# Kernel tuning notes

Hardware: AMD Instinct MI355X
Metric: run time of the kernel (lower is better)

## Reference

```python
import jax, jax.numpy as jnp
import numpy as np


def _normalize(x):
    # F.normalize(x, dim=-1): x / max(||x||_2, eps)
    n = jnp.linalg.norm(x, axis=-1, keepdims=True)
    return x / jnp.maximum(n, 1e-12)


def _clip_loss(i_sh, t_sh, scale, y):
    # Faithful, vectorized version of CLIP.forward (y: [B,1] int labels).
    i_n = _normalize(i_sh)
    t_n = _normalize(t_sh)
    logit_i2t = (i_n @ t_n.T) * scale            # [B,B]
    logit_t2i = t_n @ i_n.T                      # NOTE: no scale, as in source
    bs = i_sh.shape[0]
    yv = y.reshape(-1)                           # [B]
    # y.expand(bs,bs).T with y [bs,1] -> base[k,j] = y[j]
    base = jnp.broadcast_to(yv[None, :], (bs, bs)).astype(i_sh.dtype)
    flipped = jnp.where(base == 0, 1.0, 0.0)     # the inner loop flips 0<->nonzero
    label = jnp.where(yv[:, None] == 0, flipped, base)
    q = jax.nn.softmax(label / label.sum(axis=-1, keepdims=True), axis=-1)
    lq = jnp.log(q)
    lp1 = jax.nn.log_softmax(logit_i2t, axis=-1)
    lp2 = jax.nn.log_softmax(logit_t2i, axis=-1)
    # F.kl_div(input=log_pred, target, 'batchmean') = sum(target*(log(target)-input))/bs
    kl_p1_q = jnp.sum(q * (lq - lp1)) / bs
    kl_q_p1 = jnp.sum(jnp.exp(lp1) * (lp1 - lq)) / bs
    kl_p2_q = jnp.sum(q * (lq - lp2)) / bs
    kl_q_p2 = jnp.sum(jnp.exp(lp2) * (lp2 - lq)) / bs
    return (kl_p1_q + kl_q_p1 + kl_p2_q + kl_q_p2) / 4.0


def _forward(i, t, y, l1_w, l1_b, l2_w, l2_b, l3_w, l3_b, tl1_w, tl1_b, tl2_w, tl2_b,
             isp_w, isp_b, ish_w, ish_b, tsh_w, tsh_b, tsp_w, tsp_b,
             c1_w, c1_b, c2_w, c2_b, c3_w, c3_b, c4_w, c4_b, scale1, scale2):
    # ImgEncoder MLP head (penet backbone replaced by pooled 2048-d features;
    # dropout = identity, eval semantics)
    fi = jax.nn.relu(i @ l1_w.T + l1_b)
    fi = jax.nn.relu(fi @ l2_w.T + l2_b)
    fi = fi @ l3_w.T + l3_b                       # [B,128]
    # TabEncoder
    ft = jax.nn.relu(t @ tl1_w.T + tl1_b)
    ft = ft @ tl2_w.T + tl2_b                     # [B,128]
    loss1 = _clip_loss(fi, ft, jnp.exp(scale1), y)
    # SS heads
    i_sp = fi @ isp_w.T + isp_b
    i_sh = fi @ ish_w.T + ish_b
    t_sh = ft @ tsh_w.T + tsh_b
    t_sp = ft @ tsp_w.T + tsp_b
    # Separate: mean of Frobenius norms of BxB cross-Grams
    loss_sp = (jnp.linalg.norm(t_sp @ t_sh.T) + jnp.linalg.norm(i_sp @ i_sh.T)) / 2.0
    loss_sh = _clip_loss(i_sh, t_sh, jnp.exp(scale2), y)
    loss = (loss_sp + loss_sh + loss1) / 3.0
    i_sp_out = i_sp @ c1_w.T + c1_b
    i_sh_out = i_sh @ c2_w.T + c2_b
    t_sh_out = t_sh @ c3_w.T + c3_b
    t_sp_out = t_sp @ c4_w.T + c4_b
    return (loss, i_sp_out, i_sh_out, t_sp_out, t_sh_out)


def setup_inputs() -> dict:
    key = jax.random.key(0)
    ks = jax.random.split(key, 20)
    B = 4096

    def lin(k, out_d, in_d):  # kaiming-normal fan_out, relu
        return jax.random.normal(k, (out_d, in_d), jnp.float32) * np.sqrt(2.0 / out_d)

    log_scale = jnp.asarray(np.log(1.0 / 0.07), jnp.float32)
    return {
        'i': jax.random.normal(ks[0], (B, 2048), jnp.float32),
        't': jax.random.normal(ks[1], (B, 49), jnp.float32),
        'y': jax.random.randint(ks[2], (B, 1), 0, 2, jnp.int64 if jax.config.read('jax_enable_x64') else jnp.int32),
        'l1_w': lin(ks[3], 512, 2048), 'l1_b': jnp.zeros((512,), jnp.float32),
        'l2_w': lin(ks[4], 256, 512), 'l2_b': jnp.zeros((256,), jnp.float32),
        'l3_w': lin(ks[5], 128, 256), 'l3_b': jnp.zeros((128,), jnp.float32),
        'tl1_w': lin(ks[6], 128, 49), 'tl1_b': jnp.zeros((128,), jnp.float32),
        'tl2_w': lin(ks[7], 128, 128), 'tl2_b': jnp.zeros((128,), jnp.float32),
        'isp_w': lin(ks[8], 128, 128), 'isp_b': jnp.zeros((128,), jnp.float32),
        'ish_w': lin(ks[9], 128, 128), 'ish_b': jnp.zeros((128,), jnp.float32),
        'tsh_w': lin(ks[10], 128, 128), 'tsh_b': jnp.zeros((128,), jnp.float32),
        'tsp_w': lin(ks[11], 128, 128), 'tsp_b': jnp.zeros((128,), jnp.float32),
        'c1_w': lin(ks[12], 1, 128), 'c1_b': jnp.zeros((1,), jnp.float32),
        'c2_w': lin(ks[13], 1, 128), 'c2_b': jnp.zeros((1,), jnp.float32),
        'c3_w': lin(ks[14], 1, 128), 'c3_b': jnp.zeros((1,), jnp.float32),
        'c4_w': lin(ks[15], 1, 128), 'c4_b': jnp.zeros((1,), jnp.float32),
        'scale1': log_scale, 'scale2': log_scale,
    }


def reference(i, t, y, l1_w, l1_b, l2_w, l2_b, l3_w, l3_b, tl1_w, tl1_b, tl2_w, tl2_b,
              isp_w, isp_b, ish_w, ish_b, tsh_w, tsh_b, tsp_w, tsp_b,
              c1_w, c1_b, c2_w, c2_b, c3_w, c3_b, c4_w, c4_b, scale1, scale2):
    return _forward(i, t, y, l1_w, l1_b, l2_w, l2_b, l3_w, l3_b, tl1_w, tl1_b, tl2_w, tl2_b,
                    isp_w, isp_b, ish_w, ish_b, tsh_w, tsh_b, tsp_w, tsp_b,
                    c1_w, c1_b, c2_w, c2_b, c3_w, c3_b, c4_w, c4_b, scale1, scale2)
```

## Files before the change

kernel.cpp:

```cpp
#include <hip/hip_runtime.h>
#include <math.h>

#define BSZ 4096

typedef __attribute__((ext_vector_type(8))) short bf16x8;
typedef __attribute__((ext_vector_type(4))) float f32x4;

#define ST_ROW 0
#define ST_COL 786432
#define ST_T   1572864
#define ST_FLOATS 1589248

__device__ __forceinline__ unsigned short f2b(float f) {
    unsigned u = __float_as_uint(f);
    u = u + 0x7fffu + ((u >> 16) & 1u);
    return (unsigned short)(u >> 16);
}
__device__ __forceinline__ float b2f(unsigned short s) {
    return __uint_as_float(((unsigned)s) << 16);
}

__global__ void cast_kernel(const float* __restrict__ x, unsigned short* __restrict__ o, int n) {
    int i = (blockIdx.x * 256 + threadIdx.x) * 4;
    if (i >= n) return;
    float4 v = *(const float4*)(x + i);
    ushort4 r;
    r.x = f2b(v.x); r.y = f2b(v.y); r.z = f2b(v.z); r.w = f2b(v.w);
    *(ushort4*)(o + i) = r;
}

__global__ void cast_w_kernel(const float* __restrict__ l1, const float* __restrict__ l2,
                              const float* __restrict__ l3, const float* __restrict__ tl2,
                              const float* __restrict__ isp, const float* __restrict__ ish,
                              const float* __restrict__ tsh, const float* __restrict__ tsp,
                              unsigned short* __restrict__ o) {
    int i = (blockIdx.x * 256 + threadIdx.x) * 4;
    if (i >= 1294336) return;
    const float* src; int off;
    if (i < 1048576)      { src = l1;  off = 0; }
    else if (i < 1179648) { src = l2;  off = 1048576; }
    else if (i < 1212416) { src = l3;  off = 1179648; }
    else if (i < 1228800) { src = tl2; off = 1212416; }
    else if (i < 1245184) { src = isp; off = 1228800; }
    else if (i < 1261568) { src = ish; off = 1245184; }
    else if (i < 1277952) { src = tsh; off = 1261568; }
    else                  { src = tsp; off = 1277952; }
    float4 v = *(const float4*)(src + (i - off));
    ushort4 r;
    r.x = f2b(v.x); r.y = f2b(v.y); r.z = f2b(v.z); r.w = f2b(v.w);
    *(ushort4*)(o + i) = r;
}

__global__ void gemm_small(const float* __restrict__ A, const float* __restrict__ W,
                           const float* __restrict__ bias, unsigned short* __restrict__ C,
                           int M, int N, int K, int relu) {
    __shared__ float As[16][65];
    __shared__ float Ws[16][65];
    const int tx = threadIdx.x, ty = threadIdx.y;
    const int tid = ty * 16 + tx;
    const int m0 = blockIdx.y * 64, n0 = blockIdx.x * 64;
    float acc[4][4] = {};
    const int lrow = tid >> 2;
    const int lkb = (tid & 3) * 4;
    for (int k0 = 0; k0 < K; k0 += 16) {
#pragma unroll
        for (int u = 0; u < 4; ++u) {
            int k = k0 + lkb + u;
            As[lkb + u][lrow] = (k < K) ? A[(size_t)(m0 + lrow) * K + k] : 0.0f;
            Ws[lkb + u][lrow] = (k < K) ? W[(size_t)(n0 + lrow) * K + k] : 0.0f;
        }
        __syncthreads();
#pragma unroll
        for (int kk = 0; kk < 16; ++kk) {
            float av[4], bv[4];
#pragma unroll
            for (int i = 0; i < 4; ++i) av[i] = As[kk][ty * 4 + i];
#pragma unroll
            for (int j = 0; j < 4; ++j) bv[j] = Ws[kk][tx * 4 + j];
#pragma unroll
            for (int i = 0; i < 4; ++i)
#pragma unroll
                for (int j = 0; j < 4; ++j) acc[i][j] += av[i] * bv[j];
        }
        __syncthreads();
    }
#pragma unroll
    for (int i = 0; i < 4; ++i)
#pragma unroll
        for (int j = 0; j < 4; ++j) {
            int n = n0 + tx * 4 + j;
            float v = acc[i][j] + bias[n];
            if (relu) v = fmaxf(v, 0.0f);
            C[(size_t)(m0 + ty * 4 + i) * N + n] = f2b(v);
        }
}

__device__ __forceinline__ void gemm_body(const unsigned short* __restrict__ A,
                                          const unsigned short* __restrict__ W,
                                          const float* __restrict__ bias,
                                          unsigned short* __restrict__ Cb,
                                          float* __restrict__ Cf,
                                          int N, int K, int relu, int bx, int by,
                                          short* As, short* Bs) {
    const int tid = threadIdx.x;
    const int w = tid >> 6, lane = tid & 63, quad = lane >> 4, l15 = lane & 15;
    const int m0 = by * 128, n0 = bx * 128;
    const int rw = (w >> 1) * 64, cw = (w & 1) * 64;
    f32x4 acc[4][4];
#pragma unroll
    for (int i = 0; i < 4; ++i)
#pragma unroll
        for (int j = 0; j < 4; ++j) acc[i][j] = (f32x4){0.f, 0.f, 0.f, 0.f};

    for (int k0 = 0; k0 < K; k0 += 64) {
#pragma unroll
        for (int r = 0; r < 4; ++r) {
            int idx = r * 256 + tid;
            int row = idx >> 3, cbp = idx & 7;
            int col = ((cbp ^ (row & 7)) << 3);
            *(bf16x8*)&As[row * 64 + cbp * 8] = *(const bf16x8*)&A[(size_t)(m0 + row) * K + k0 + col];
            *(bf16x8*)&Bs[row * 64 + cbp * 8] = *(const bf16x8*)&W[(size_t)(n0 + row) * K + k0 + col];
        }
        __syncthreads();
#pragma unroll
        for (int kb = 0; kb < 2; ++kb) {
            bf16x8 af[4], bfr[4];
            int cb = kb * 4 + quad;
#pragma unroll
            for (int i = 0; i < 4; ++i) {
                int row = rw + i * 16 + l15;
                af[i] = *(const bf16x8*)&As[row * 64 + ((cb ^ (row & 7)) << 3)];
            }
#pragma unroll
            for (int j = 0; j < 4; ++j) {
                int row = cw + j * 16 + l15;
                bfr[j] = *(const bf16x8*)&Bs[row * 64 + ((cb ^ (row & 7)) << 3)];
            }
#pragma unroll
            for (int i = 0; i < 4; ++i)
#pragma unroll
                for (int j = 0; j < 4; ++j)
                    acc[i][j] = __builtin_amdgcn_mfma_f32_16x16x32_bf16(af[i], bfr[j], acc[i][j], 0, 0, 0);
        }
        __syncthreads();
    }
#pragma unroll
    for (int j = 0; j < 4; ++j) {
        int n = n0 + cw + j * 16 + l15;
        float bv = bias[n];
#pragma unroll
        for (int i = 0; i < 4; ++i) {
#pragma unroll
            for (int r = 0; r < 4; ++r) {
                int m = m0 + rw + i * 16 + quad * 4 + r;
                float v = acc[i][j][r] + bv;
                if (relu) v = fmaxf(v, 0.f);
                if (Cb) Cb[(size_t)m * N + n] = f2b(v);
                if (Cf) Cf[(size_t)m * N + n] = v;
            }
        }
    }
}

__global__ __launch_bounds__(256) void mfma_gemm(const unsigned short* __restrict__ A,
                                                 const unsigned short* __restrict__ W,
                                                 const float* __restrict__ bias,
                                                 unsigned short* __restrict__ Cb,
                                                 float* __restrict__ Cf, int N, int K, int relu) {
    __shared__ alignas(16) short As[128 * 64];
    __shared__ alignas(16) short Bs[128 * 64];
    gemm_body(A, W, bias, Cb, Cf, N, K, relu, blockIdx.x, blockIdx.y, As, Bs);
}

__global__ __launch_bounds__(256) void mfma_heads(const unsigned short* __restrict__ FIb,
                                                  const unsigned short* __restrict__ FTb,
                                                  const unsigned short* __restrict__ Wisp,
                                                  const unsigned short* __restrict__ Wish,
                                                  const unsigned short* __restrict__ Wtsh,
                                                  const unsigned short* __restrict__ Wtsp,
                                                  const float* __restrict__ bisp, const float* __restrict__ bish,
                                                  const float* __restrict__ btsh, const float* __restrict__ btsp,
                                                  float* __restrict__ ISP, float* __restrict__ ISH,
                                                  float* __restrict__ TSH, float* __restrict__ TSP) {
    __shared__ alignas(16) short As[128 * 64];
    __shared__ alignas(16) short Bs[128 * 64];
    int z = blockIdx.z;
    const unsigned short* A = (z < 2) ? FIb : FTb;
    const unsigned short* W = z == 0 ? Wisp : z == 1 ? Wish : z == 2 ? Wtsh : Wtsp;
    const float* b = z == 0 ? bisp : z == 1 ? bish : z == 2 ? btsh : btsp;
    float* C = z == 0 ? ISP : z == 1 ? ISH : z == 2 ? TSH : TSP;
    gemm_body(A, W, b, nullptr, C, 128, 128, 0, 0, blockIdx.y, As, Bs);
}

__global__ void rownorm4(const unsigned short* __restrict__ fi, const unsigned short* __restrict__ ft,
                         const float* __restrict__ ish, const float* __restrict__ tsh,
                         unsigned short* __restrict__ fin, unsigned short* __restrict__ ftn,
                         unsigned short* __restrict__ ishn, unsigned short* __restrict__ tshn) {
    int z = blockIdx.y;
    int m = blockIdx.x * 256 + threadIdx.x;
    const unsigned short* sb = (z == 0) ? fi : ft;
    const float* sf = (z == 2) ? ish : tsh;
    unsigned short* dst = z == 0 ? fin : z == 1 ? ftn : z == 2 ? ishn : tshn;
    float ss = 0.f;
    if (z < 2) {
        for (int u = 0; u < 128; u += 8) {
            bf16x8 v = *(const bf16x8*)&sb[(size_t)m * 128 + u];
#pragma unroll
            for (int e = 0; e < 8; ++e) { float f = b2f((unsigned short)v[e]); ss += f * f; }
        }
    } else {
        for (int u = 0; u < 128; u += 4) {
            float4 v = *(const float4*)&sf[(size_t)m * 128 + u];
            ss += v.x * v.x + v.y * v.y + v.z * v.z + v.w * v.w;
        }
    }
    float inv = 1.f / fmaxf(sqrtf(ss), 1e-12f);
    if (z < 2) {
        for (int u = 0; u < 128; u += 8) {
            bf16x8 v = *(const bf16x8*)&sb[(size_t)m * 128 + u];
            ushort4 o0, o1;
            o0.x = f2b(b2f((unsigned short)v[0]) * inv); o0.y = f2b(b2f((unsigned short)v[1]) * inv);
            o0.z = f2b(b2f((unsigned short)v[2]) * inv); o0.w = f2b(b2f((unsigned short)v[3]) * inv);
            o1.x = f2b(b2f((unsigned short)v[4]) * inv); o1.y = f2b(b2f((unsigned short)v[5]) * inv);
            o1.z = f2b(b2f((unsigned short)v[6]) * inv); o1.w = f2b(b2f((unsigned short)v[7]) * inv);
            *(ushort4*)&dst[(size_t)m * 128 + u] = o0;
            *(ushort4*)&dst[(size_t)m * 128 + u + 4] = o1;
        }
    } else {
        for (int u = 0; u < 128; u += 4) {
            float4 v = *(const float4*)&sf[(size_t)m * 128 + u];
            ushort4 o;
            o.x = f2b(v.x * inv); o.y = f2b(v.y * inv); o.z = f2b(v.z * inv); o.w = f2b(v.w * inv);
            *(ushort4*)&dst[(size_t)m * 128 + u] = o;
        }
    }
}

__global__ __launch_bounds__(256) void clip_mfma(const unsigned short* __restrict__ In1,
                                                 const unsigned short* __restrict__ Tn1,
                                                 const unsigned short* __restrict__ In2,
                                                 const unsigned short* __restrict__ Tn2,
                                                 const int* __restrict__ y,
                                                 const float* __restrict__ scale_log1,
                                                 const float* __restrict__ scale_log2,
                                                 float* __restrict__ st1, float* __restrict__ st2) {
    __shared__ alignas(16) short As[128 * 128];
    __shared__ alignas(16) short Bs[128 * 128];
    const int z = blockIdx.z;
    const unsigned short* In = z ? In2 : In1;
    const unsigned short* Tn = z ? Tn2 : Tn1;
    const float* scale_log = z ? scale_log2 : scale_log1;
    float* st = z ? st2 : st1;
    const int tid = threadIdx.x;
    const int w = tid >> 6, lane = tid & 63, quad = lane >> 4, l15 = lane & 15;
    const int bx = blockIdx.x, by = blockIdx.y;
    const int r0 = by * 128, c0 = bx * 128;
    const int rw = (w >> 1) * 64, cw = (w & 1) * 64;
#pragma unroll
    for (int r = 0; r < 8; ++r) {
        int idx = r * 256 + tid;
        int row = idx >> 4, cbp = idx & 15;
        int col = ((cbp ^ (row & 7)) << 3);
        *(bf16x8*)&As[row * 128 + cbp * 8] = *(const bf16x8*)&In[(size_t)(r0 + row) * 128 + col];
        *(bf16x8*)&Bs[row * 128 + cbp * 8] = *(const bf16x8*)&Tn[(size_t)(c0 + row) * 128 + col];
    }
    __syncthreads();
    f32x4 acc[4][4];
#pragma unroll
    for (int i = 0; i < 4; ++i)
#pragma unroll
        for (int j = 0; j < 4; ++j) acc[i][j] = (f32x4){0.f, 0.f, 0.f, 0.f};
#pragma unroll
    for (int kb = 0; kb < 4; ++kb) {
        bf16x8 af[4], bfr[4];
        int cb = kb * 4 + quad;
#pragma unroll
        for (int i = 0; i < 4; ++i) {
            int row = rw + i * 16 + l15;
            af[i] = *(const bf16x8*)&As[row * 128 + ((cb ^ (row & 7)) << 3)];
        }
#pragma unroll
        for (int j = 0; j < 4; ++j) {
            int row = cw + j * 16 + l15;
            bfr[j] = *(const bf16x8*)&Bs[row * 128 + ((cb ^ (row & 7)) << 3)];
        }
#pragma unroll
        for (int i = 0; i < 4; ++i)
#pragma unroll
            for (int j = 0; j < 4; ++j)
                acc[i][j] = __builtin_amdgcn_mfma_f32_16x16x32_bf16(af[i], bfr[j], acc[i][j], 0, 0, 0);
    }

    const float s = expf(scale_log[0]);
    int yrow[4][4]; float mrow[4][4];
    int ycol[4];    float mcol[4];
#pragma unroll
    for (int i = 0; i < 4; ++i)
#pragma unroll
        for (int r = 0; r < 4; ++r) {
            int yy = y[r0 + rw + i * 16 + quad * 4 + r];
            yrow[i][r] = yy; mrow[i][r] = (yy == 0) ? 1.f : 0.f;
        }
#pragma unroll
    for (int j = 0; j < 4; ++j) {
        int yy = y[c0 + cw + j * 16 + l15];
        ycol[j] = yy; mcol[j] = (yy == 0) ? 1.f : 0.f;
    }
    float rZ[4][4] = {}, rF[4][4] = {}, rW[4][4] = {};
    float cZ[4] = {}, cE[4] = {}, cW[4] = {};
    float aAll = 0.f, aC0 = 0.f, aR0 = 0.f, aRC = 0.f;
#pragma unroll
    for (int i = 0; i < 4; ++i)
#pragma unroll
        for (int r = 0; r < 4; ++r) {
            float mr = mrow[i][r];
            int yr = yrow[i][r];
#pragma unroll
            for (int j = 0; j < 4; ++j) {
                float S = acc[i][j][r];
                float L = s * S;
                float e1 = __expf(L);
                float e2 = __expf(S);
                float msk = (yr == ycol[j]) ? 1.f : 0.f;
                rZ[i][r] += e1; rF[i][r] += e1 * L; rW[i][r] += e1 * msk;
                cZ[j] += e2;    cE[j] += e2 * S;    cW[j] += e2 * msk;
                float tmp = S * mcol[j];
                aAll += S; aC0 += tmp; aR0 += S * mr; aRC += tmp * mr;
            }
        }
    const int p_row = bx * 2 + (cw >> 6);
#pragma unroll
    for (int i = 0; i < 4; ++i)
#pragma unroll
        for (int r = 0; r < 4; ++r) {
#pragma unroll
            for (int m = 1; m < 16; m <<= 1) {
                rZ[i][r] += __shfl_xor(rZ[i][r], m);
                rF[i][r] += __shfl_xor(rF[i][r], m);
                rW[i][r] += __shfl_xor(rW[i][r], m);
            }
            if (l15 == (i * 4 + r)) {
                int grow = r0 + rw + i * 16 + quad * 4 + r;
                int base = ST_ROW + p_row * 4096 + grow;
                st[base]          = rZ[i][r];
                st[base + 262144] = rF[i][r];
                st[base + 524288] = rW[i][r];
            }
        }
    const int p_col = by * 2 + (rw >> 6);
#pragma unroll
    for (int j = 0; j < 4; ++j) {
        cZ[j] += __shfl_xor(cZ[j], 16); cZ[j] += __shfl_xor(cZ[j], 32);
        cE[j] += __shfl_xor(cE[j], 16); cE[j] += __shfl_xor(cE[j], 32);
        cW[j] += __shfl_xor(cW[j], 16); cW[j] += __shfl_xor(cW[j], 32);
        if (quad == 0) {
            int gcol = c0 + cw + j * 16 + l15;
            int base = ST_COL + p_col * 4096 + gcol;
            st[base]          = cZ[j];
            st[base + 262144] = cE[j];
            st[base + 524288] = cW[j];
        }
    }
#pragma unroll
    for (int m = 1; m < 64; m <<= 1) {
        aAll += __shfl_xor(aAll, m); aC0 += __shfl_xor(aC0, m);
        aR0 += __shfl_xor(aR0, m);   aRC += __shfl_xor(aRC, m);
    }
    if (lane == 0) {
        int wg = (by * 32 + bx) * 4 + w;
        float T00 = aRC, T01 = aR0 - aRC, T10 = aC0 - aRC, T11 = aAll - aR0 - aC0 + aRC;
        st[ST_T + wg * 4 + 0] = T00;
        st[ST_T + wg * 4 + 1] = T01;
        st[ST_T + wg * 4 + 2] = T10;
        st[ST_T + wg * 4 + 3] = T11;
    }
}

__global__ void clip_finalize(const float* __restrict__ st1, const float* __restrict__ st2,
                              const int* __restrict__ y,
                              const float* __restrict__ scale_log1, const float* __restrict__ scale_log2,
                              float* __restrict__ loss_base) {
    __shared__ float red[256];
    __shared__ float4 tred[256];
    const int z = blockIdx.y;
    const float* st = z ? st2 : st1;
    const float* scale_log = z ? scale_log2 : scale_log1;
    float* loss_slot = loss_base + z;
    int tid = threadIdx.x;
    int k = blockIdx.x * 256 + tid;
    const float Bf = (float)BSZ;

    float ccnt = 0.f;
    for (int i = tid; i < BSZ; i += 256) ccnt += (y[i] == 0) ? 1.f : 0.f;
    red[tid] = ccnt;
    __syncthreads();
    for (int ss2 = 128; ss2 > 0; ss2 >>= 1) {
        if (tid < ss2) red[tid] += red[tid + ss2];
        __syncthreads();
    }
    const float n0 = red[0];
    __syncthreads();

    int yk = y[k];
    float n = (yk == 0) ? n0 : (Bf - n0);
    float a = 1.0f / n;
    float ea = expf(a);
    float denom = n * ea + (Bf - n);
    float q_s = ea / denom, q_d = 1.0f / denom;
    float ld = logf(denom);
    float lq_s = a - ld, lq_d = -ld;
    float Qlq = n * q_s * lq_s + (Bf - n) * q_d * lq_d;

    float Z1 = 0.f, F1 = 0.f, W1 = 0.f, Z2 = 0.f, E2 = 0.f, W2 = 0.f;
#pragma unroll 8
    for (int p = 0; p < 64; ++p) {
        int base = p * 4096 + k;
        Z1 += st[ST_ROW + base];
        F1 += st[ST_ROW + base + 262144];
        W1 += st[ST_ROW + base + 524288];
        Z2 += st[ST_COL + base];
        E2 += st[ST_COL + base + 262144];
        W2 += st[ST_COL + base + 524288];
    }
    float term_r = Qlq + F1 / Z1 - lq_d - (lq_s - lq_d) * (W1 / Z1);
    float term_c = Qlq + E2 / Z2 - lq_d - (lq_s - lq_d) * (W2 / Z2);
    float v = (term_r + term_c) / (4.0f * Bf);
    red[tid] = v;

    if (blockIdx.x == 0) {
        const float4* tp = (const float4*)&st[ST_T];
        float4 acc = {0.f, 0.f, 0.f, 0.f};
        for (int u = tid; u < 4096; u += 256) {
            float4 t4 = tp[u];
            acc.x += t4.x; acc.y += t4.y; acc.z += t4.z; acc.w += t4.w;
        }
        tred[tid] = acc;
    }
    __syncthreads();
    for (int ss2 = 128; ss2 > 0; ss2 >>= 1) {
        if (tid < ss2) {
            red[tid] += red[tid + ss2];
            if (blockIdx.x == 0) {
                tred[tid].x += tred[tid + ss2].x; tred[tid].y += tred[tid + ss2].y;
                tred[tid].z += tred[tid + ss2].z; tred[tid].w += tred[tid + ss2].w;
            }
        }
        __syncthreads();
    }
    if (tid == 0) {
        float total = red[0];
        if (blockIdx.x == 0) {
            const float s = expf(scale_log[0]);
            float n1 = Bf - n0;
            float a0 = 1.f / n0, a1 = 1.f / n1;
            float e0 = expf(a0), e1 = expf(a1);
            float d0 = n0 * e0 + (Bf - n0), d1 = n1 * e1 + (Bf - n1);
            float qs0 = e0 / d0, qd0 = 1.f / d0, qs1 = e1 / d1, qd1 = 1.f / d1;
            float T00 = tred[0].x, T01 = tred[0].y, T10 = tred[0].z, T11 = tred[0].w;
            float QS1 = qd0 * (T00 + T01) + (qs0 - qd0) * T00 + qd1 * (T10 + T11) + (qs1 - qd1) * T11;
            float QS2 = qd0 * (T00 + T10) + (qs0 - qd0) * T00 + qd1 * (T01 + T11) + (qs1 - qd1) * T11;
            total += (-s * QS1 - QS2) / (4.0f * Bf);
        }
        atomicAdd(loss_slot, total);
    }
}

__global__ __launch_bounds__(256) void gram_splitk(const float* __restrict__ isp,
                                                   const float* __restrict__ ish,
                                                   const float* __restrict__ tsp,
                                                   const float* __restrict__ tsh,
                                                   float* __restrict__ GP) {
    __shared__ alignas(16) float As2[64][128];
    const int mat = blockIdx.y, chunk = blockIdx.x;
    const float* A = mat == 0 ? isp : mat == 1 ? ish : mat == 2 ? tsp : tsh;
    const int tid = threadIdx.x;
    const int m0 = chunk * 64;
#pragma unroll
    for (int r = 0; r < 8; ++r) {
        int idx = r * 256 + tid;
        int row = idx >> 5, c4 = (idx & 31) * 4;
        *(float4*)&As2[row][c4] = *(const float4*)&A[(size_t)(m0 + row) * 128 + c4];
    }
    __syncthreads();
    const int ty = tid >> 4, tx = tid & 15;
    float acc[8][8] = {};
    for (int k = 0; k < 64; ++k) {
        float av[8], bv[8];
        *(float4*)&av[0] = *(const float4*)&As2[k][ty * 8];
        *(float4*)&av[4] = *(const float4*)&As2[k][ty * 8 + 4];
        *(float4*)&bv[0] = *(const float4*)&As2[k][tx * 8];
        *(float4*)&bv[4] = *(const float4*)&As2[k][tx * 8 + 4];
#pragma unroll
        for (int i = 0; i < 8; ++i)
#pragma unroll
            for (int j = 0; j < 8; ++j) acc[i][j] += av[i] * bv[j];
    }
    float* Gp = GP + ((size_t)(mat * 64 + chunk) << 14);
#pragma unroll
    for (int i = 0; i < 8; ++i) {
        *(float4*)&Gp[(ty * 8 + i) * 128 + tx * 8]     = *(float4*)&acc[i][0];
        *(float4*)&Gp[(ty * 8 + i) * 128 + tx * 8 + 4] = *(float4*)&acc[i][4];
    }
}

__global__ void frob_combine(const float* __restrict__ GP, float* __restrict__ scal) {
    __shared__ float red[256];
    const int z = blockIdx.y;
    const int tid = threadIdx.x;
    int u = blockIdx.x * 1024 + tid * 4;
    float4 ga = {0.f, 0.f, 0.f, 0.f};
    float4 gb = {0.f, 0.f, 0.f, 0.f};
    const size_t baseA = ((size_t)(2 * z) * 64) << 14;
    const size_t baseB = ((size_t)(2 * z + 1) * 64) << 14;
    for (int c = 0; c < 64; ++c) {
        float4 va = *(const float4*)&GP[baseA + ((size_t)c << 14) + u];
        float4 vb = *(const float4*)&GP[baseB + ((size_t)c << 14) + u];
        ga.x += va.x; ga.y += va.y; ga.z += va.z; ga.w += va.w;
        gb.x += vb.x; gb.y += vb.y; gb.z += vb.z; gb.w += vb.w;
    }
    red[tid] = ga.x * gb.x + ga.y * gb.y + ga.z * gb.z + ga.w * gb.w;
    __syncthreads();
    for (int ss = 128; ss > 0; ss >>= 1) {
        if (tid < ss) red[tid] += red[tid + ss];
        __syncthreads();
    }
    if (tid == 0) atomicAdd(&scal[3 + z], red[0]);
}

__global__ void head4(const float* __restrict__ isp, const float* __restrict__ ish,
                      const float* __restrict__ tsp, const float* __restrict__ tsh,
                      const float* __restrict__ c1w, const float* __restrict__ c2w,
                      const float* __restrict__ c4w, const float* __restrict__ c3w,
                      const float* __restrict__ c1b, const float* __restrict__ c2b,
                      const float* __restrict__ c4b, const float* __restrict__ c3b,
                      float* __restrict__ out) {
    int z = blockIdx.y;
    const float* X = z == 0 ? isp : z == 1 ? ish : z == 2 ? tsp : tsh;
    const float* w = z == 0 ? c1w : z == 1 ? c2w : z == 2 ? c4w : c3w;
    const float* b = z == 0 ? c1b : z == 1 ? c2b : z == 2 ? c4b : c3b;
    int m = blockIdx.x * 256 + threadIdx.x;
    const float4* xp = (const float4*)(X + (size_t)m * 128);
    const float4* wp = (const float4*)w;
    float acc = 0.0f;
#pragma unroll
    for (int u = 0; u < 32; ++u) {
        float4 av = xp[u], cv = wp[u];
        acc += av.x * cv.x + av.y * cv.y + av.z * cv.z + av.w * cv.w;
    }
    out[1 + (size_t)z * BSZ + m] = acc + b[0];
}

__global__ void final_kernel(const float* __restrict__ scal, float* __restrict__ out) {
    float loss1 = scal[1];
    float loss_sh = scal[2];
    float ss_i = scal[3];
    float ss_t = scal[4];
    float loss_sp = 0.5f * (sqrtf(ss_t) + sqrtf(ss_i));
    out[0] = (loss_sp + loss_sh + loss1) / 3.0f;
}

extern "C" void kernel_launch(void* const* d_in, const int* in_sizes, int n_in,
                              void* d_out, int out_size, void* d_ws, size_t ws_size,
                              hipStream_t stream) {
    const float* i_in  = (const float*)d_in[0];
    const float* t_in  = (const float*)d_in[1];
    const int*   y     = (const int*)d_in[2];
    const float* l1_w  = (const float*)d_in[3];
    const float* l1_b  = (const float*)d_in[4];
    const float* l2_w  = (const float*)d_in[5];
    const float* l2_b  = (const float*)d_in[6];
    const float* l3_w  = (const float*)d_in[7];
    const float* l3_b  = (const float*)d_in[8];
    const float* tl1_w = (const float*)d_in[9];
    const float* tl1_b = (const float*)d_in[10];
    const float* tl2_w = (const float*)d_in[11];
    const float* tl2_b = (const float*)d_in[12];
    const float* isp_w = (const float*)d_in[13];
    const float* isp_b = (const float*)d_in[14];
    const float* ish_w = (const float*)d_in[15];
    const float* ish_b = (const float*)d_in[16];
    const float* tsh_w = (const float*)d_in[17];
    const float* tsh_b = (const float*)d_in[18];
    const float* tsp_w = (const float*)d_in[19];
    const float* tsp_b = (const float*)d_in[20];
    const float* c1_w  = (const float*)d_in[21];
    const float* c1_b  = (const float*)d_in[22];
    const float* c2_w  = (const float*)d_in[23];
    const float* c2_b  = (const float*)d_in[24];
    const float* c3_w  = (const float*)d_in[25];
    const float* c3_b  = (const float*)d_in[26];
    const float* c4_w  = (const float*)d_in[27];
    const float* c4_b  = (const float*)d_in[28];
    const float* scale1 = (const float*)d_in[29];
    const float* scale2 = (const float*)d_in[30];

    float* ws = (float*)d_ws;
    float* SCAL = ws;
    float* ISP  = ws + 64;
    float* ISH  = ISP + (size_t)BSZ * 128;
    float* TSP  = ISH + (size_t)BSZ * 128;
    float* TSH  = TSP + (size_t)BSZ * 128;
    unsigned short* IB   = (unsigned short*)(TSH + (size_t)BSZ * 128);
    unsigned short* WB   = IB + (size_t)BSZ * 2048;
    unsigned short* FI1B = WB + 1294336;
    unsigned short* FI2B = FI1B + (size_t)BSZ * 512;
    unsigned short* FIB  = FI2B + (size_t)BSZ * 256;
    unsigned short* FT1B = FIB + (size_t)BSZ * 128;
    unsigned short* FTB  = FT1B + (size_t)BSZ * 128;
    unsigned short* FINB = FTB + (size_t)BSZ * 128;
    unsigned short* FTNB = FINB + (size_t)BSZ * 128;
    unsigned short* ISHN = FTNB + (size_t)BSZ * 128;
    unsigned short* TSHN = ISHN + (size_t)BSZ * 128;
    float* ST1 = (float*)IB;
    float* ST2 = ST1 + ST_FLOATS;
    float* GP = (float*)IB;

    float* out = (float*)d_out;

    hipMemsetAsync(d_ws, 0, 64 * sizeof(float), stream);
    cast_kernel<<<8192, 256, 0, stream>>>(i_in, IB, BSZ * 2048);
    cast_w_kernel<<<1264, 256, 0, stream>>>(l1_w, l2_w, l3_w, tl2_w, isp_w, ish_w, tsh_w, tsp_w, WB);
    gemm_small<<<dim3(2, 64), dim3(16, 16), 0, stream>>>(t_in, tl1_w, tl1_b, FT1B, BSZ, 128, 49, 1);

    mfma_gemm<<<dim3(4, 32), 256, 0, stream>>>(IB, WB, l1_b, FI1B, nullptr, 512, 2048, 1);
    mfma_gemm<<<dim3(2, 32), 256, 0, stream>>>(FI1B, WB + 1048576, l2_b, FI2B, nullptr, 256, 512, 1);
    mfma_gemm<<<dim3(1, 32), 256, 0, stream>>>(FI2B, WB + 1179648, l3_b, FIB, nullptr, 128, 256, 0);
    mfma_gemm<<<dim3(1, 32), 256, 0, stream>>>(FT1B, WB + 1212416, tl2_b, FTB, nullptr, 128, 128, 0);
    mfma_heads<<<dim3(1, 32, 4), 256, 0, stream>>>(FIB, FTB, WB + 1228800, WB + 1245184, WB + 1261568,
                                                   WB + 1277952, isp_b, ish_b, tsh_b, tsp_b,
                                                   ISP, ISH, TSH, TSP);
    rownorm4<<<dim3(16, 4), 256, 0, stream>>>(FIB, FTB, ISH, TSH, FINB, FTNB, ISHN, TSHN);

    clip_mfma<<<dim3(32, 32, 2), 256, 0, stream>>>(FINB, FTNB, ISHN, TSHN, y, scale1, scale2, ST1, ST2);
    clip_finalize<<<dim3(16, 2), 256, 0, stream>>>(ST1, ST2, y, scale1, scale2, &SCAL[1]);

    gram_splitk<<<dim3(64, 4), 256, 0, stream>>>(ISP, ISH, TSP, TSH, GP);
    frob_combine<<<dim3(16, 2), 256, 0, stream>>>(GP, SCAL);
    head4<<<dim3(16, 4), 256, 0, stream>>>(ISP, ISH, TSP, TSH, c1_w, c2_w, c4_w, c3_w,
                                           c1_b, c2_b, c4_b, c3_b, out);
    final_kernel<<<1, 1, 0, stream>>>(SCAL, out);
}
```

Before: 350.6 us.

## Split CLIP K-loop into halves, transpose-reduce stats, and parallelize finalize

The clip_mfma kernel now stages K in two 64-wide chunks, halving LDS use to raise occupancy. Its row and column statistic reductions use a butterfly transpose-reduce, so each lane writes one value instead of running full shuffle trees for every row. clip_finalize is widened to one wavefront per row, with a wave-level shuffle reduction over the 64 partials, and it no longer recounts y==0 in every block. That count moves to a separate small kernel, and the final combine (plus the former atomics) moves into a 256-thread final_kernel. The cost is extra launches, an extra sync in the K loop, and an extra RV buffer in the workspace.

```diff
diff --git a/kernel.cpp b/kernel.cpp
--- a/kernel.cpp
+++ b/kernel.cpp
@@ -236,6 +236,20 @@
     }
 }
 
+__global__ void county_kernel(const int* __restrict__ y, float* __restrict__ scal) {
+    __shared__ int red[256];
+    int t = threadIdx.x;
+    int c = 0;
+    for (int i = t; i < BSZ; i += 256) c += (y[i] == 0) ? 1 : 0;
+    red[t] = c;
+    __syncthreads();
+    for (int s = 128; s > 0; s >>= 1) {
+        if (t < s) red[t] += red[t + s];
+        __syncthreads();
+    }
+    if (t == 0) scal[0] = (float)red[0];
+}
+
 __global__ __launch_bounds__(256) void clip_mfma(const unsigned short* __restrict__ In1,
                                                  const unsigned short* __restrict__ Tn1,
                                                  const unsigned short* __restrict__ In2,
@@ -244,8 +258,8 @@
                                                  const float* __restrict__ scale_log1,
                                                  const float* __restrict__ scale_log2,
                                                  float* __restrict__ st1, float* __restrict__ st2) {
-    __shared__ alignas(16) short As[128 * 128];
-    __shared__ alignas(16) short Bs[128 * 128];
+    __shared__ alignas(16) short As[128 * 64];
+    __shared__ alignas(16) short Bs[128 * 64];
     const int z = blockIdx.z;
     const unsigned short* In = z ? In2 : In1;
     const unsigned short* Tn = z ? Tn2 : Tn1;
@@ -256,39 +270,42 @@
     const int bx = blockIdx.x, by = blockIdx.y;
     const int r0 = by * 128, c0 = bx * 128;
     const int rw = (w >> 1) * 64, cw = (w & 1) * 64;
-#pragma unroll
-    for (int r = 0; r < 8; ++r) {
-        int idx = r * 256 + tid;
-        int row = idx >> 4, cbp = idx & 15;
-        int col = ((cbp ^ (row & 7)) << 3);
-        *(bf16x8*)&As[row * 128 + cbp * 8] = *(const bf16x8*)&In[(size_t)(r0 + row) * 128 + col];
-        *(bf16x8*)&Bs[row * 128 + cbp * 8] = *(const bf16x8*)&Tn[(size_t)(c0 + row) * 128 + col];
-    }
-    __syncthreads();
     f32x4 acc[4][4];
 #pragma unroll
     for (int i = 0; i < 4; ++i)
 #pragma unroll
         for (int j = 0; j < 4; ++j) acc[i][j] = (f32x4){0.f, 0.f, 0.f, 0.f};
-#pragma unroll
-    for (int kb = 0; kb < 4; ++kb) {
-        bf16x8 af[4], bfr[4];
-        int cb = kb * 4 + quad;
-#pragma unroll
-        for (int i = 0; i < 4; ++i) {
-            int row = rw + i * 16 + l15;
-            af[i] = *(const bf16x8*)&As[row * 128 + ((cb ^ (row & 7)) << 3)];
-        }
-#pragma unroll
-        for (int j = 0; j < 4; ++j) {
-            int row = cw + j * 16 + l15;
-            bfr[j] = *(const bf16x8*)&Bs[row * 128 + ((cb ^ (row & 7)) << 3)];
-        }
-#pragma unroll
-        for (int i = 0; i < 4; ++i)
-#pragma unroll
-            for (int j = 0; j < 4; ++j)
-                acc[i][j] = __builtin_amdgcn_mfma_f32_16x16x32_bf16(af[i], bfr[j], acc[i][j], 0, 0, 0);
+    for (int k0 = 0; k0 < 128; k0 += 64) {
+#pragma unroll
+        for (int r = 0; r < 4; ++r) {
+            int idx = r * 256 + tid;
+            int row = idx >> 3, cbp = idx & 7;
+            int col = ((cbp ^ (row & 7)) << 3);
+            *(bf16x8*)&As[row * 64 + cbp * 8] = *(const bf16x8*)&In[(size_t)(r0 + row) * 128 + k0 + col];
+            *(bf16x8*)&Bs[row * 64 + cbp * 8] = *(const bf16x8*)&Tn[(size_t)(c0 + row) * 128 + k0 + col];
+        }
+        __syncthreads();
+#pragma unroll
+        for (int kb = 0; kb < 2; ++kb) {
+            bf16x8 af[4], bfr[4];
+            int cb = kb * 4 + quad;
+#pragma unroll
+            for (int i = 0; i < 4; ++i) {
+                int row = rw + i * 16 + l15;
+                af[i] = *(const bf16x8*)&As[row * 64 + ((cb ^ (row & 7)) << 3)];
+            }
+#pragma unroll
+            for (int j = 0; j < 4; ++j) {
+                int row = cw + j * 16 + l15;
+                bfr[j] = *(const bf16x8*)&Bs[row * 64 + ((cb ^ (row & 7)) << 3)];
+            }
+#pragma unroll
+            for (int i = 0; i < 4; ++i)
+#pragma unroll
+                for (int j = 0; j < 4; ++j)
+                    acc[i][j] = __builtin_amdgcn_mfma_f32_16x16x32_bf16(af[i], bfr[j], acc[i][j], 0, 0, 0);
+        }
+        __syncthreads();
     }
 
     const float s = expf(scale_log[0]);
@@ -306,13 +323,16 @@
         int yy = y[c0 + cw + j * 16 + l15];
         ycol[j] = yy; mcol[j] = (yy == 0) ? 1.f : 0.f;
     }
-    float rZ[4][4] = {}, rF[4][4] = {}, rW[4][4] = {};
+    float vZ[16], vF[16], vW[16];
+#pragma unroll
+    for (int q = 0; q < 16; ++q) { vZ[q] = 0.f; vF[q] = 0.f; vW[q] = 0.f; }
     float cZ[4] = {}, cE[4] = {}, cW[4] = {};
     float aAll = 0.f, aC0 = 0.f, aR0 = 0.f, aRC = 0.f;
 #pragma unroll
     for (int i = 0; i < 4; ++i)
 #pragma unroll
         for (int r = 0; r < 4; ++r) {
+            const int idx = i * 4 + r;
             float mr = mrow[i][r];
             int yr = yrow[i][r];
 #pragma unroll
@@ -322,44 +342,60 @@
                 float e1 = __expf(L);
                 float e2 = __expf(S);
                 float msk = (yr == ycol[j]) ? 1.f : 0.f;
-                rZ[i][r] += e1; rF[i][r] += e1 * L; rW[i][r] += e1 * msk;
-                cZ[j] += e2;    cE[j] += e2 * S;    cW[j] += e2 * msk;
+                vZ[idx] += e1; vF[idx] += e1 * L; vW[idx] += e1 * msk;
+                cZ[j] += e2;   cE[j] += e2 * S;   cW[j] += e2 * msk;
                 float tmp = S * mcol[j];
                 aAll += S; aC0 += tmp; aR0 += S * mr; aRC += tmp * mr;
             }
         }
-    const int p_row = bx * 2 + (cw >> 6);
-#pragma unroll
-    for (int i = 0; i < 4; ++i)
-#pragma unroll
-        for (int r = 0; r < 4; ++r) {
-#pragma unroll
-            for (int m = 1; m < 16; m <<= 1) {
-                rZ[i][r] += __shfl_xor(rZ[i][r], m);
-                rF[i][r] += __shfl_xor(rF[i][r], m);
-                rW[i][r] += __shfl_xor(rW[i][r], m);
-            }
-            if (l15 == (i * 4 + r)) {
-                int grow = r0 + rw + i * 16 + quad * 4 + r;
-                int base = ST_ROW + p_row * 4096 + grow;
-                st[base]          = rZ[i][r];
-                st[base + 262144] = rF[i][r];
-                st[base + 524288] = rW[i][r];
-            }
-        }
-    const int p_col = by * 2 + (rw >> 6);
-#pragma unroll
-    for (int j = 0; j < 4; ++j) {
-        cZ[j] += __shfl_xor(cZ[j], 16); cZ[j] += __shfl_xor(cZ[j], 32);
-        cE[j] += __shfl_xor(cE[j], 16); cE[j] += __shfl_xor(cE[j], 32);
-        cW[j] += __shfl_xor(cW[j], 16); cW[j] += __shfl_xor(cW[j], 32);
-        if (quad == 0) {
-            int gcol = c0 + cw + j * 16 + l15;
-            int base = ST_COL + p_col * 4096 + gcol;
-            st[base]          = cZ[j];
-            st[base + 262144] = cE[j];
-            st[base + 524288] = cW[j];
-        }
+#pragma unroll
+    for (int b = 8; b >= 1; b >>= 1) {
+        const bool hi = (l15 & b) != 0;
+#pragma unroll
+        for (int j = 0; j < b; ++j) {
+            float sZ = hi ? vZ[j] : vZ[j + b];
+            float kZ = hi ? vZ[j + b] : vZ[j];
+            vZ[j] = kZ + __shfl_xor(sZ, b);
+            float sF = hi ? vF[j] : vF[j + b];
+            float kF = hi ? vF[j + b] : vF[j];
+            vF[j] = kF + __shfl_xor(sF, b);
+            float sW = hi ? vW[j] : vW[j + b];
+            float kW = hi ? vW[j + b] : vW[j];
+            vW[j] = kW + __shfl_xor(sW, b);
+        }
+    }
+    {
+        const int p_row = bx * 2 + (cw >> 6);
+        int grow = r0 + rw + (l15 >> 2) * 16 + quad * 4 + (l15 & 3);
+        int base = ST_ROW + p_row * 4096 + grow;
+        st[base]          = vZ[0];
+        st[base + 262144] = vF[0];
+        st[base + 524288] = vW[0];
+    }
+#pragma unroll
+    for (int b = 2; b >= 1; b >>= 1) {
+        const int lm = b << 4;
+        const bool hi = (lane & lm) != 0;
+#pragma unroll
+        for (int j = 0; j < b; ++j) {
+            float sZ = hi ? cZ[j] : cZ[j + b];
+            float kZ = hi ? cZ[j + b] : cZ[j];
+            cZ[j] = kZ + __shfl_xor(sZ, lm);
+            float sE = hi ? cE[j] : cE[j + b];
+            float kE = hi ? cE[j + b] : cE[j];
+            cE[j] = kE + __shfl_xor(sE, lm);
+            float sW = hi ? cW[j] : cW[j + b];
+            float kW = hi ? cW[j + b] : cW[j];
+            cW[j] = kW + __shfl_xor(sW, lm);
+        }
+    }
+    {
+        const int p_col = by * 2 + (rw >> 6);
+        int gcol = c0 + cw + quad * 16 + l15;
+        int base = ST_COL + p_col * 4096 + gcol;
+        st[base]          = cZ[0];
+        st[base + 262144] = cE[0];
+        st[base + 524288] = cW[0];
     }
 #pragma unroll
     for (int m = 1; m < 64; m <<= 1) {
@@ -376,58 +412,47 @@
     }
 }
 
-__global__ void clip_finalize(const float* __restrict__ st1, const float* __restrict__ st2,
-                              const int* __restrict__ y,
-                              const float* __restrict__ scale_log1, const float* __restrict__ scale_log2,
-                              float* __restrict__ loss_base) {
-    __shared__ float red[256];
-    __shared__ float4 tred[256];
+__global__ __launch_bounds__(256) void clip_finalize(const float* __restrict__ st1,
+                                                     const float* __restrict__ st2,
+                                                     const int* __restrict__ y,
+                                                     const float* __restrict__ scal,
+                                                     float* __restrict__ RV,
+                                                     float* __restrict__ TT) {
     const int z = blockIdx.y;
     const float* st = z ? st2 : st1;
-    const float* scale_log = z ? scale_log2 : scale_log1;
-    float* loss_slot = loss_base + z;
-    int tid = threadIdx.x;
-    int k = blockIdx.x * 256 + tid;
+    const int tid = threadIdx.x;
+    const int lane = tid & 63;
+    const int k = blockIdx.x * 4 + (tid >> 6);
     const float Bf = (float)BSZ;
-
-    float ccnt = 0.f;
-    for (int i = tid; i < BSZ; i += 256) ccnt += (y[i] == 0) ? 1.f : 0.f;
-    red[tid] = ccnt;
-    __syncthreads();
-    for (int ss2 = 128; ss2 > 0; ss2 >>= 1) {
-        if (tid < ss2) red[tid] += red[tid + ss2];
-        __syncthreads();
-    }
-    const float n0 = red[0];
-    __syncthreads();
-
-    int yk = y[k];
-    float n = (yk == 0) ? n0 : (Bf - n0);
-    float a = 1.0f / n;
-    float ea = expf(a);
-    float denom = n * ea + (Bf - n);
-    float q_s = ea / denom, q_d = 1.0f / denom;
-    float ld = logf(denom);
-    float lq_s = a - ld, lq_d = -ld;
-    float Qlq = n * q_s * lq_s + (Bf - n) * q_d * lq_d;
-
-    float Z1 = 0.f, F1 = 0.f, W1 = 0.f, Z2 = 0.f, E2 = 0.f, W2 = 0.f;
-#pragma unroll 8
-    for (int p = 0; p < 64; ++p) {
-        int base = p * 4096 + k;
-        Z1 += st[ST_ROW + base];
-        F1 += st[ST_ROW + base + 262144];
-        W1 += st[ST_ROW + base + 524288];
-        Z2 += st[ST_COL + base];
-        E2 += st[ST_COL + base + 262144];
-        W2 += st[ST_COL + base + 524288];
-    }
-    float term_r = Qlq + F1 / Z1 - lq_d - (lq_s - lq_d) * (W1 / Z1);
-    float term_c = Qlq + E2 / Z2 - lq_d - (lq_s - lq_d) * (W2 / Z2);
-    float v = (term_r + term_c) / (4.0f * Bf);
-    red[tid] = v;
-
+    const int base = lane * 4096 + k;
+    float Z1 = st[ST_ROW + base];
+    float F1 = st[ST_ROW + 262144 + base];
+    float W1 = st[ST_ROW + 524288 + base];
+    float Z2 = st[ST_COL + base];
+    float E2 = st[ST_COL + 262144 + base];
+    float W2 = st[ST_COL + 524288 + base];
+#pragma unroll
+    for (int m = 1; m < 64; m <<= 1) {
+        Z1 += __shfl_xor(Z1, m); F1 += __shfl_xor(F1, m); W1 += __shfl_xor(W1, m);
+        Z2 += __shfl_xor(Z2, m); E2 += __shfl_xor(E2, m); W2 += __shfl_xor(W2, m);
+    }
+    if (lane == 0) {
+        float n0 = scal[0];
+        int yk = y[k];
+        float n = (yk == 0) ? n0 : (Bf - n0);
+        float a = 1.0f / n;
+        float ea = expf(a);
+        float denom = n * ea + (Bf - n);
+        float q_s = ea / denom, q_d = 1.0f / denom;
+        float ld = logf(denom);
+        float lq_s = a - ld, lq_d = -ld;
+        float Qlq = n * q_s * lq_s + (Bf - n) * q_d * lq_d;
+        float term_r = Qlq + F1 / Z1 - lq_d - (lq_s - lq_d) * (W1 / Z1);
+        float term_c = Qlq + E2 / Z2 - lq_d - (lq_s - lq_d) * (W2 / Z2);
+        RV[(size_t)z * BSZ + k] = (term_r + term_c) / (4.0f * Bf);
+    }
     if (blockIdx.x == 0) {
+        __shared__ float4 tred[256];
         const float4* tp = (const float4*)&st[ST_T];
         float4 acc = {0.f, 0.f, 0.f, 0.f};
         for (int u = tid; u < 4096; u += 256) {
@@ -435,33 +460,18 @@
             acc.x += t4.x; acc.y += t4.y; acc.z += t4.z; acc.w += t4.w;
         }
         tred[tid] = acc;
-    }
-    __syncthreads();
-    for (int ss2 = 128; ss2 > 0; ss2 >>= 1) {
-        if (tid < ss2) {
-            red[tid] += red[tid + ss2];
-            if (blockIdx.x == 0) {
+        __syncthreads();
+        for (int ss2 = 128; ss2 > 0; ss2 >>= 1) {
+            if (tid < ss2) {
                 tred[tid].x += tred[tid + ss2].x; tred[tid].y += tred[tid + ss2].y;
                 tred[tid].z += tred[tid + ss2].z; tred[tid].w += tred[tid + ss2].w;
             }
-        }
-        __syncthreads();
-    }
-    if (tid == 0) {
-        float total = red[0];
-        if (blockIdx.x == 0) {
-            const float s = expf(scale_log[0]);
-            float n1 = Bf - n0;
-            float a0 = 1.f / n0, a1 = 1.f / n1;
-            float e0 = expf(a0), e1 = expf(a1);
-            float d0 = n0 * e0 + (Bf - n0), d1 = n1 * e1 + (Bf - n1);
-            float qs0 = e0 / d0, qd0 = 1.f / d0, qs1 = e1 / d1, qd1 = 1.f / d1;
-            float T00 = tred[0].x, T01 = tred[0].y, T10 = tred[0].z, T11 = tred[0].w;
-            float QS1 = qd0 * (T00 + T01) + (qs0 - qd0) * T00 + qd1 * (T10 + T11) + (qs1 - qd1) * T11;
-            float QS2 = qd0 * (T00 + T10) + (qs0 - qd0) * T00 + qd1 * (T01 + T11) + (qs1 - qd1) * T11;
-            total += (-s * QS1 - QS2) / (4.0f * Bf);
-        }
-        atomicAdd(loss_slot, total);
+            __syncthreads();
+        }
+        if (tid == 0) {
+            TT[z * 4 + 0] = tred[0].x; TT[z * 4 + 1] = tred[0].y;
+            TT[z * 4 + 2] = tred[0].z; TT[z * 4 + 3] = tred[0].w;
+        }
     }
 }
 
@@ -550,13 +560,37 @@
     out[1 + (size_t)z * BSZ + m] = acc + b[0];
 }
 
-__global__ void final_kernel(const float* __restrict__ scal, float* __restrict__ out) {
-    float loss1 = scal[1];
-    float loss_sh = scal[2];
-    float ss_i = scal[3];
-    float ss_t = scal[4];
-    float loss_sp = 0.5f * (sqrtf(ss_t) + sqrtf(ss_i));
-    out[0] = (loss_sp + loss_sh + loss1) / 3.0f;
+__global__ void final_kernel(const float* __restrict__ RV, const float* __restrict__ scal,
+                             const float* __restrict__ sl1, const float* __restrict__ sl2,
+                             float* __restrict__ out) {
+    __shared__ float red0[256], red1[256];
+    int tid = threadIdx.x;
+    float s0 = 0.f, s1 = 0.f;
+    for (int u = tid; u < BSZ; u += 256) { s0 += RV[u]; s1 += RV[BSZ + u]; }
+    red0[tid] = s0; red1[tid] = s1;
+    __syncthreads();
+    for (int ss = 128; ss > 0; ss >>= 1) {
+        if (tid < ss) { red0[tid] += red0[tid + ss]; red1[tid] += red1[tid + ss]; }
+        __syncthreads();
+    }
+    if (tid == 0) {
+        const float Bf = (float)BSZ;
+        float n0 = scal[0], n1 = Bf - n0;
+        float e0 = expf(1.f / n0), e1 = expf(1.f / n1);
+        float d0 = n0 * e0 + (Bf - n0), d1 = n1 * e1 + (Bf - n1);
+        float qs0 = e0 / d0, qd0 = 1.f / d0, qs1 = e1 / d1, qd1 = 1.f / d1;
+        float loss_z[2];
+        for (int z = 0; z < 2; ++z) {
+            float T00 = scal[8 + z * 4 + 0], T01 = scal[8 + z * 4 + 1];
+            float T10 = scal[8 + z * 4 + 2], T11 = scal[8 + z * 4 + 3];
+            float QS1 = qd0 * (T00 + T01) + (qs0 - qd0) * T00 + qd1 * (T10 + T11) + (qs1 - qd1) * T11;
+            float QS2 = qd0 * (T00 + T10) + (qs0 - qd0) * T00 + qd1 * (T01 + T11) + (qs1 - qd1) * T11;
+            float s = expf(z ? sl2[0] : sl1[0]);
+            loss_z[z] = (z ? red1[0] : red0[0]) + (-s * QS1 - QS2) / (4.0f * Bf);
+        }
+        float loss_sp = 0.5f * (sqrtf(scal[4]) + sqrtf(scal[3]));
+        out[0] = (loss_sp + loss_z[1] + loss_z[0]) / 3.0f;
+    }
 }
 
 extern "C" void kernel_launch(void* const* d_in, const int* in_sizes, int n_in,
@@ -596,7 +630,8 @@
 
     float* ws = (float*)d_ws;
     float* SCAL = ws;
-    float* ISP  = ws + 64;
+    float* RV   = ws + 64;
+    float* ISP  = RV + 2 * BSZ;
     float* ISH  = ISP + (size_t)BSZ * 128;
     float* TSP  = ISH + (size_t)BSZ * 128;
     float* TSH  = TSP + (size_t)BSZ * 128;
@@ -618,6 +653,7 @@
     float* out = (float*)d_out;
 
     hipMemsetAsync(d_ws, 0, 64 * sizeof(float), stream);
+    county_kernel<<<1, 256, 0, stream>>>(y, SCAL);
     cast_kernel<<<8192, 256, 0, stream>>>(i_in, IB, BSZ * 2048);
     cast_w_kernel<<<1264, 256, 0, stream>>>(l1_w, l2_w, l3_w, tl2_w, isp_w, ish_w, tsh_w, tsp_w, WB);
     gemm_small<<<dim3(2, 64), dim3(16, 16), 0, stream>>>(t_in, tl1_w, tl1_b, FT1B, BSZ, 128, 49, 1);
@@ -632,11 +668,11 @@
     rownorm4<<<dim3(16, 4), 256, 0, stream>>>(FIB, FTB, ISH, TSH, FINB, FTNB, ISHN, TSHN);
 
     clip_mfma<<<dim3(32, 32, 2), 256, 0, stream>>>(FINB, FTNB, ISHN, TSHN, y, scale1, scale2, ST1, ST2);
-    clip_finalize<<<dim3(16, 2), 256, 0, stream>>>(ST1, ST2, y, scale1, scale2, &SCAL[1]);
+    clip_finalize<<<dim3(1024, 2), 256, 0, stream>>>(ST1, ST2, y, SCAL, RV, &SCAL[8]);
 
     gram_splitk<<<dim3(64, 4), 256, 0, stream>>>(ISP, ISH, TSP, TSH, GP);
     frob_combine<<<dim3(16, 2), 256, 0, stream>>>(GP, SCAL);
     head4<<<dim3(16, 4), 256, 0, stream>>>(ISP, ISH, TSP, TSH, c1_w, c2_w, c4_w, c3_w,
                                            c1_b, c2_b, c4_b, c3_b, out);
-    final_kernel<<<1, 1, 0, stream>>>(SCAL, out);
-}
+    final_kernel<<<1, 256, 0, stream>>>(RV, SCAL, scale1, scale2, out);
+}
```

Measured after the change: 485.5 us. +38.4%, slower.
